# Optimization experiments

Measured on AMD Instinct MI355X. Metric: run time of the kernel, lower is better.

The kernel has to match this reference:

```python
import jax, jax.numpy as jnp
import numpy as np
import math

DIM = 4096
N_HEADS = 32
HEAD_DIM = DIM // N_HEADS  # 128


def setup_inputs() -> dict:
    key = jax.random.key(0)
    ks = jax.random.split(key, 10)
    B, S, C = 2, 1024, 2048
    x = jax.random.normal(ks[0], (B, S, DIM), dtype=jnp.float32)
    freqs_cis = jax.random.normal(ks[1], (S, HEAD_DIM // 2), dtype=jnp.float32)
    mask = jnp.zeros((1, 1, S, C), dtype=jnp.float32)
    input_idexes = jnp.arange(S, dtype=jnp.int64) if jax.config.jax_enable_x64 else jnp.arange(S, dtype=jnp.int32)
    cache_k = jax.random.normal(ks[2], (B, C, N_HEADS, HEAD_DIM), dtype=jnp.float32) * 0.1
    cache_v = jax.random.normal(ks[3], (B, C, N_HEADS, HEAD_DIM), dtype=jnp.float32) * 0.1
    # Linear weights in torch layout [out_features, in_features], y = x @ W.T
    wq = jax.random.normal(ks[4], (DIM, DIM), dtype=jnp.float32) * 0.02
    wk = jax.random.normal(ks[5], (DIM, DIM), dtype=jnp.float32) * 0.02
    wv = jax.random.normal(ks[6], (DIM, DIM), dtype=jnp.float32) * 0.02
    wo = jax.random.normal(ks[7], (DIM, DIM), dtype=jnp.float32) * 0.02
    return {"x": x, "freqs_cis": freqs_cis, "mask": mask, "input_idexes": input_idexes,
            "cache_k": cache_k, "cache_v": cache_v, "wq": wq, "wk": wk, "wv": wv, "wo": wo}


def reference(x, freqs_cis, mask, input_idexes, cache_k, cache_v, wq, wk, wv, wo):
    B, S, D = x.shape
    H, hd = N_HEADS, HEAD_DIM
    # projections (torch Linear: x @ W.T)
    xq = jnp.einsum('bsd,ed->bse', x, wq).reshape(B, S, H, hd)
    # xk/xv are computed in the original forward but never used (cache-only attention)
    xk = jnp.einsum('bsd,ed->bse', x, wk).reshape(B, S, H, hd)  # noqa: F841
    xv = jnp.einsum('bsd,ed->bse', x, wv).reshape(B, S, H, hd)  # noqa: F841
    q = xq.transpose(0, 2, 1, 3)                 # [B,H,S,hd]
    keys = cache_k.transpose(0, 2, 1, 3)         # [B,H,C,hd]
    values = cache_v.transpose(0, 2, 1, 3)       # [B,H,C,hd]
    scores = jnp.einsum('bhse,bhce->bhsc', q, keys) / math.sqrt(hd)
    scores = scores + mask
    attn = jax.nn.softmax(scores.astype(jnp.float32), axis=-1).astype(q.dtype)
    out = jnp.einsum('bhsc,bhce->bhse', attn, values)  # [B,H,S,hd]
    out = out.transpose(0, 2, 1, 3).reshape(B, S, H * hd)
    return jnp.einsum('bse,de->bsd', out, wo)
```

## Files before the change

kernel.cpp:

```cpp
#include <hip/hip_runtime.h>
#include <hip/hip_bf16.h>
#include <stdint.h>


#define DIM   4096
#define NH    32
#define HD    128
#define BB    2
#define SS    1024
#define CC    2048

typedef __bf16 bf16x8 __attribute__((ext_vector_type(8)));
typedef float  f32x4  __attribute__((ext_vector_type(4)));

__device__ __forceinline__ unsigned short f2bf(float f) {
  union { __hip_bfloat16 h; unsigned short u; } cv;
  cv.h = __float2bfloat16(f);
  return cv.u;
}

__device__ __forceinline__ void gl_lds16(const void* g, void* l) {
  __builtin_amdgcn_global_load_lds(
      (__attribute__((address_space(1))) void*)(uintptr_t)(g),
      (__attribute__((address_space(3))) void*)(l), 16, 0, 0);
}

__global__ void conv_f32_bf16(const float* __restrict__ in, unsigned short* __restrict__ out, int n4) {
  int i = blockIdx.x * blockDim.x + threadIdx.x;
  int stride = gridDim.x * blockDim.x;
  for (; i < n4; i += stride) {
    float4 v = reinterpret_cast<const float4*>(in)[i];
    ushort4 o;
    o.x = f2bf(v.x); o.y = f2bf(v.y); o.z = f2bf(v.z); o.w = f2bf(v.w);
    reinterpret_cast<ushort4*>(out)[i] = o;
  }
}

__global__ __launch_bounds__(256) void prep_a(
    const float* __restrict__ x,  unsigned short* __restrict__ xbf,
    const float* __restrict__ wq, unsigned short* __restrict__ wbf)
{
  const int b = blockIdx.x, t = threadIdx.x;
  const float* in; unsigned short* out; int base, nthr, n4;
  if (b < 1024) { in = x;  out = xbf; base = b;        nthr = 1024 * 256; n4 = BB * SS * DIM / 4; }
  else          { in = wq; out = wbf; base = b - 1024; nthr = 2048 * 256; n4 = DIM * DIM / 4; }
  for (int i = base * 256 + t; i < n4; i += nthr) {
    float4 v = reinterpret_cast<const float4*>(in)[i];
    ushort4 o;
    o.x = f2bf(v.x); o.y = f2bf(v.y); o.z = f2bf(v.z); o.w = f2bf(v.w);
    reinterpret_cast<ushort4*>(out)[i] = o;
  }
}

__global__ __launch_bounds__(256) void prep_b(
    const float* __restrict__ ck,  unsigned short* __restrict__ kbf,
    const float* __restrict__ cv,  unsigned short* __restrict__ vtbf,
    const float* __restrict__ mask, int* __restrict__ flags)
{
  const int b = blockIdx.x, t = threadIdx.x;

  if (b < 2048) {
    const int total4 = BB * NH * CC * HD / 4;
    for (int i = b * 256 + t; i < total4; i += 2048 * 256) {
      size_t o = (size_t)i * 4;
      int d  = (int)(o & (HD - 1));
      size_t r = o >> 7;
      int c  = (int)(r & (CC - 1));
      int bh = (int)(r >> 11);
      int hh = bh & (NH - 1), bb = bh >> 5;
      float4 v = *reinterpret_cast<const float4*>(ck + ((size_t)(bb * CC + c) * NH + hh) * HD + d);
      ushort4 u; u.x = f2bf(v.x); u.y = f2bf(v.y); u.z = f2bf(v.z); u.w = f2bf(v.w);
      *reinterpret_cast<ushort4*>(kbf + o) = u;
    }
  } else if (b < 6144) {
    __shared__ float tile[64][65];
    const int e  = b - 2048;
    const int ct = e & 31, rest = e >> 5;
    const int dt = rest & 1, bh = rest >> 1;
    const int hh = bh & (NH - 1), bb = bh >> 5;
    const int c0 = ct * 64, d0 = dt * 64;
    const int tx = t & 63, ty = t >> 6;
#pragma unroll
    for (int i = 0; i < 16; ++i) {
      int cl = ty + i * 4;
      tile[cl][tx] = cv[((size_t)(bb * CC + c0 + cl) * NH + hh) * HD + d0 + tx];
    }
    __syncthreads();
    const int c4 = (t & 15) * 4, dr = t >> 4;
#pragma unroll
    for (int i = 0; i < 4; ++i) {
      int dl = dr + i * 16;
      ushort4 o;
      o.x = f2bf(tile[c4 + 0][dl]); o.y = f2bf(tile[c4 + 1][dl]);
      o.z = f2bf(tile[c4 + 2][dl]); o.w = f2bf(tile[c4 + 3][dl]);
      *reinterpret_cast<ushort4*>(&vtbf[((size_t)bh * HD + d0 + dl) * CC + c0 + c4]) = o;
    }
  } else {
    __shared__ int s[4];
    const int e  = b - 6144;
    const int qt = e >> 5, ct = e & 31;
    const int w = t >> 6;
    const float4* m4 = (const float4*)mask;
    int nz = 0;
#pragma unroll
    for (int i = 0; i < 8; ++i) {
      int idx = i * 256 + t;
      int row = idx >> 4, c4 = idx & 15;
      float4 v = m4[(size_t)(qt * 128 + row) * (CC / 4) + ct * 16 + c4];
      nz |= (v.x != 0.f) | (v.y != 0.f) | (v.z != 0.f) | (v.w != 0.f);
    }
    int wa = (int)__any(nz);
    if ((t & 63) == 0) s[w] = wa;
    __syncthreads();
    if (t == 0) flags[qt * 32 + ct] = s[0] | s[1] | s[2] | s[3];
  }
}

template <int OUT_BF16>
__global__ __launch_bounds__(256, 2) void gemm_bt(
    const unsigned short* __restrict__ A,
    const unsigned short* __restrict__ Bw,
    void* __restrict__ Cout,
    int M, int N, int K, float scale)
{
  __shared__ __align__(16) unsigned short As[128 * 32];
  __shared__ __align__(16) unsigned short Bs[128 * 32];
  const int t = threadIdx.x;
  const int w = t >> 6, lane = t & 63;
  const int wr = w >> 1, wc = w & 1;
  const int bm0 = blockIdx.y * 128, bn0 = blockIdx.x * 128;

  const unsigned short* aSrc = A  + (size_t)(bm0 + (t >> 2)) * K + (t & 3) * 8;
  const unsigned short* bSrc = Bw + (size_t)(bn0 + (t >> 2)) * K + (t & 3) * 8;
  char* aDst = (char*)As + w * 1024;
  char* bDst = (char*)Bs + w * 1024;
  const size_t half = (size_t)64 * K;

  f32x4 acc[4][4];
#pragma unroll
  for (int m = 0; m < 4; ++m)
#pragma unroll
    for (int n = 0; n < 4; ++n) acc[m][n] = (f32x4){0.f, 0.f, 0.f, 0.f};

  for (int k0 = 0; k0 < K; k0 += 32) {
    gl_lds16(aSrc,        aDst);
    gl_lds16(aSrc + half, aDst + 4096);
    gl_lds16(bSrc,        bDst);
    gl_lds16(bSrc + half, bDst + 4096);
    aSrc += 32; bSrc += 32;
    __syncthreads();

    bf16x8 af[4], bf[4];
#pragma unroll
    for (int m = 0; m < 4; ++m)
      af[m] = *(const bf16x8*)&As[(wr * 64 + m * 16 + (lane & 15)) * 32 + (lane >> 4) * 8];
#pragma unroll
    for (int n = 0; n < 4; ++n)
      bf[n] = *(const bf16x8*)&Bs[(wc * 64 + n * 16 + (lane & 15)) * 32 + (lane >> 4) * 8];
#pragma unroll
    for (int m = 0; m < 4; ++m)
#pragma unroll
      for (int n = 0; n < 4; ++n)
        acc[m][n] = __builtin_amdgcn_mfma_f32_16x16x32_bf16(af[m], bf[n], acc[m][n], 0, 0, 0);
    __syncthreads();
  }

  const int r0 = (lane >> 4) * 4, cl = lane & 15;
#pragma unroll
  for (int m = 0; m < 4; ++m) {
#pragma unroll
    for (int n = 0; n < 4; ++n) {
      int row = bm0 + wr * 64 + m * 16 + r0;
      int col = bn0 + wc * 64 + n * 16 + cl;
#pragma unroll
      for (int r = 0; r < 4; ++r) {
        float v = acc[m][n][r] * scale;
        if (OUT_BF16) ((unsigned short*)Cout)[(size_t)(row + r) * N + col] = f2bf(v);
        else          ((float*)Cout)[(size_t)(row + r) * N + col] = v;
      }
    }
  }
}

__global__ __launch_bounds__(256, 2) void fused_qattn(
    const unsigned short* __restrict__ Ax,
    const unsigned short* __restrict__ Wq,
    const unsigned short* __restrict__ Kb,
    const unsigned short* __restrict__ Vtb,
    const float* __restrict__ mask,
    const int* __restrict__ Mf,
    unsigned short* __restrict__ Ob)
{
  __shared__ __align__(16) unsigned short SM[40960];

  const int t = threadIdx.x, w = t >> 6, lane = t & 63;
  const int lg = (blockIdx.x & 7) * 64 + (blockIdx.x >> 3);
  const int qt = lg & 7, bh = lg >> 3;
  const int hh = bh & (NH - 1), bb = bh >> 5;
  const int q0 = qt * 128;
  const int l15 = lane & 15, g = lane >> 4;
  const int rb4 = g * 4;
  const int wr = w >> 1, wc = w & 1;

  const int bm0 = bb * SS + q0;
  const int bn0 = hh * HD;
  {
    unsigned short* As = SM;
    unsigned short* Bs = SM + 4096;
    const unsigned short* aSrc = Ax + (size_t)(bm0 + (t >> 2)) * DIM + (t & 3) * 8;
    const unsigned short* bSrc = Wq + (size_t)(bn0 + (t >> 2)) * DIM + (t & 3) * 8;
    char* aDst = (char*)As + w * 1024;
    char* bDst = (char*)Bs + w * 1024;
    const size_t half = (size_t)64 * DIM;

    f32x4 acc[4][4];
#pragma unroll
    for (int m = 0; m < 4; ++m)
#pragma unroll
      for (int n = 0; n < 4; ++n) acc[m][n] = (f32x4){0.f, 0.f, 0.f, 0.f};

    for (int k0 = 0; k0 < DIM; k0 += 32) {
      gl_lds16(aSrc,        aDst);
      gl_lds16(aSrc + half, aDst + 4096);
      gl_lds16(bSrc,        bDst);
      gl_lds16(bSrc + half, bDst + 4096);
      aSrc += 32; bSrc += 32;
      __syncthreads();

      bf16x8 af[4], bf[4];
#pragma unroll
      for (int m = 0; m < 4; ++m)
        af[m] = *(const bf16x8*)&As[(wr * 64 + m * 16 + l15) * 32 + g * 8];
#pragma unroll
      for (int n = 0; n < 4; ++n)
        bf[n] = *(const bf16x8*)&Bs[(wc * 64 + n * 16 + l15) * 32 + g * 8];
#pragma unroll
      for (int m = 0; m < 4; ++m)
#pragma unroll
        for (int n = 0; n < 4; ++n)
          acc[m][n] = __builtin_amdgcn_mfma_f32_16x16x32_bf16(af[m], bf[n], acc[m][n], 0, 0, 0);
      __syncthreads();
    }

    const float qscale = 0.12751744682f;
    const int r0 = g * 4;
#pragma unroll
    for (int m = 0; m < 4; ++m) {
#pragma unroll
      for (int n = 0; n < 4; ++n) {
        int rl = wr * 64 + m * 16 + r0;
        int cl2 = wc * 64 + n * 16 + l15;
#pragma unroll
        for (int r = 0; r < 4; ++r) {
          int row = rl + r;
          SM[(row * 128 + cl2) ^ ((row & 7) << 3)] = f2bf(acc[m][n][r] * qscale);
        }
      }
    }
  }
  __syncthreads();

  const int swz = (lane & 7) << 3;
  bf16x8 qf[2][4];
#pragma unroll
  for (int rf = 0; rf < 2; ++rf) {
    int row = w * 32 + rf * 16 + l15;
#pragma unroll
    for (int kk = 0; kk < 4; ++kk)
      qf[rf][kk] = *(const bf16x8*)&SM[(row * 128 + kk * 32 + g * 8) ^ swz];
  }
  __syncthreads();

  unsigned short* PsW = SM + 32768 + w * 2048;

  const unsigned short* kSrc = Kb + ((size_t)bh * CC + (t >> 4)) * HD
                               + (((t & 15) ^ ((t >> 4) & 7)) * 8);
  const unsigned short* vSrc = Vtb + ((size_t)bh * HD + (t >> 3)) * CC
                               + (((t & 7) ^ ((t >> 3) & 7)) * 8);

  f32x4 acc_o[2][8];
#pragma unroll
  for (int rf = 0; rf < 2; ++rf)
#pragma unroll
    for (int i = 0; i < 8; ++i) acc_o[rf][i] = (f32x4){0.f, 0.f, 0.f, 0.f};
  float m_run[2][4], l_run[2][4];
#pragma unroll
  for (int rf = 0; rf < 2; ++rf)
#pragma unroll
    for (int r = 0; r < 4; ++r) { m_run[rf][r] = -1e30f; l_run[rf][r] = 0.f; }

  const float LOG2E = 1.4426950408889634f;

  int mflag = Mf[qt * 32];
  {
    char* kd = (char*)(SM)         + w * 1024;
    char* vd = (char*)(SM + 16384) + w * 1024;
#pragma unroll
    for (int i = 0; i < 4; ++i) {
      gl_lds16(kSrc + (size_t)(i * 16) * HD, kd + i * 4096);
      gl_lds16(vSrc + (size_t)i * 32 * CC,   vd + i * 4096);
    }
  }
  __syncthreads();

  int cur = 0;
  for (int c0 = 0; c0 < CC; c0 += 64) {
    const int ct = c0 >> 6;
    int nextFlag = (ct < 31) ? Mf[qt * 32 + ct + 1] : 0;
    unsigned short* KsC = SM + cur * 8192;
    unsigned short* VsC = SM + 16384 + cur * 8192;

    float mk[2][4][4];
    if (mflag) {
#pragma unroll
      for (int rf = 0; rf < 2; ++rf)
#pragma unroll
        for (int nf = 0; nf < 4; ++nf)
#pragma unroll
          for (int r = 0; r < 4; ++r)
            mk[rf][nf][r] = mask[(size_t)(q0 + w * 32 + rf * 16 + rb4 + r) * CC
                                 + c0 + nf * 16 + l15];
      __builtin_amdgcn_sched_barrier(0);
    }

    if (c0 + 64 < CC) {
      char* kd = (char*)(SM + (cur ^ 1) * 8192)         + w * 1024;
      char* vd = (char*)(SM + 16384 + (cur ^ 1) * 8192) + w * 1024;
#pragma unroll
      for (int i = 0; i < 4; ++i) {
        gl_lds16(kSrc + (size_t)(c0 + 64 + i * 16) * HD, kd + i * 4096);
        gl_lds16(vSrc + (size_t)i * 32 * CC + c0 + 64,   vd + i * 4096);
      }
    }
    __builtin_amdgcn_sched_barrier(0);

    f32x4 sc[2][4];
#pragma unroll
    for (int rf = 0; rf < 2; ++rf)
#pragma unroll
      for (int nf = 0; nf < 4; ++nf) sc[rf][nf] = (f32x4){0.f, 0.f, 0.f, 0.f};
    __builtin_amdgcn_s_setprio(1);
#pragma unroll
    for (int kk = 0; kk < 4; ++kk) {
#pragma unroll
      for (int nf = 0; nf < 4; ++nf) {
        bf16x8 kf = *(const bf16x8*)&KsC[((nf * 16 + l15) * 128 + kk * 32 + g * 8) ^ swz];
        sc[0][nf] = __builtin_amdgcn_mfma_f32_16x16x32_bf16(qf[0][kk], kf, sc[0][nf], 0, 0, 0);
        sc[1][nf] = __builtin_amdgcn_mfma_f32_16x16x32_bf16(qf[1][kk], kf, sc[1][nf], 0, 0, 0);
      }
    }
    __builtin_amdgcn_s_setprio(0);

    if (mflag) {
#pragma unroll
      for (int rf = 0; rf < 2; ++rf)
#pragma unroll
        for (int nf = 0; nf < 4; ++nf)
#pragma unroll
          for (int r = 0; r < 4; ++r)
            sc[rf][nf][r] = fmaf(mk[rf][nf][r], LOG2E, sc[rf][nf][r]);
    }

#pragma unroll
    for (int rf = 0; rf < 2; ++rf) {
      int ok = 1;
      float pm[4];
#pragma unroll
      for (int r = 0; r < 4; ++r) {
        pm[r] = fmaxf(fmaxf(sc[rf][0][r], sc[rf][1][r]), fmaxf(sc[rf][2][r], sc[rf][3][r]));
        ok = ok && (pm[r] <= m_run[rf][r] + 8.0f);
      }
      if (!__all(ok)) {
#pragma unroll
        for (int r = 0; r < 4; ++r) {
          float mx = pm[r];
#pragma unroll
          for (int d = 1; d < 16; d <<= 1)
            mx = fmaxf(mx, __shfl_xor(mx, d));
          float mn = fmaxf(m_run[rf][r], mx);
          float corr = __builtin_amdgcn_exp2f(m_run[rf][r] - mn);
          m_run[rf][r] = mn;
          l_run[rf][r] *= corr;
#pragma unroll
          for (int nd = 0; nd < 8; ++nd) acc_o[rf][nd][r] *= corr;
        }
      }

#pragma unroll
      for (int r = 0; r < 4; ++r) {
        int rw = rf * 16 + rb4 + r;
        int rsw = (rw & 7) << 3;
#pragma unroll
        for (int nf = 0; nf < 4; ++nf) {
          float p = __builtin_amdgcn_exp2f(sc[rf][nf][r] - m_run[rf][r]);
          l_run[rf][r] += p;
          PsW[rw * 64 + ((nf * 16 + l15) ^ rsw)] = f2bf(p);
        }
      }
    }

    __builtin_amdgcn_s_setprio(1);
#pragma unroll
    for (int kk = 0; kk < 2; ++kk) {
      bf16x8 pf0 = *(const bf16x8*)&PsW[((0 * 16 + l15) * 64 + kk * 32 + g * 8) ^ swz];
      bf16x8 pf1 = *(const bf16x8*)&PsW[((1 * 16 + l15) * 64 + kk * 32 + g * 8) ^ swz];
#pragma unroll
      for (int nd = 0; nd < 8; ++nd) {
        bf16x8 vf = *(const bf16x8*)&VsC[((nd * 16 + l15) * 64 + kk * 32 + g * 8) ^ swz];
        acc_o[0][nd] = __builtin_amdgcn_mfma_f32_16x16x32_bf16(pf0, vf, acc_o[0][nd], 0, 0, 0);
        acc_o[1][nd] = __builtin_amdgcn_mfma_f32_16x16x32_bf16(pf1, vf, acc_o[1][nd], 0, 0, 0);
      }
    }
    __builtin_amdgcn_s_setprio(0);
    __syncthreads();
    cur ^= 1;
    mflag = nextFlag;
  }

#pragma unroll
  for (int rf = 0; rf < 2; ++rf) {
#pragma unroll
    for (int r = 0; r < 4; ++r)
#pragma unroll
      for (int d = 1; d < 16; d <<= 1)
        l_run[rf][r] += __shfl_xor(l_run[rf][r], d);

#pragma unroll
    for (int nd = 0; nd < 8; ++nd)
#pragma unroll
      for (int r = 0; r < 4; ++r) {
        float v = acc_o[rf][nd][r] / l_run[rf][r];
        int row = q0 + w * 32 + rf * 16 + rb4 + r;
        Ob[(size_t)(bb * SS + row) * DIM + hh * HD + nd * 16 + l15] = f2bf(v);
      }
  }
}

extern "C" void kernel_launch(void* const* d_in, const int* in_sizes, int n_in,
                              void* d_out, int out_size, void* d_ws, size_t ws_size,
                              hipStream_t stream) {
  const float* x       = (const float*)d_in[0];
  const float* mask    = (const float*)d_in[2];
  const float* cache_k = (const float*)d_in[4];
  const float* cache_v = (const float*)d_in[5];
  const float* wq      = (const float*)d_in[6];
  const float* wo      = (const float*)d_in[9];
  float* out = (float*)d_out;

  char* ws = (char*)d_ws;
  unsigned short* Wbf  = (unsigned short*)(ws);
  unsigned short* xbf  = (unsigned short*)(ws + 33554432);
  unsigned short* qbf  = (unsigned short*)(ws + 33554432 + 16777216);
  unsigned short* kbf  = (unsigned short*)(ws + 33554432 + 2 * 16777216);
  unsigned short* vtbf = (unsigned short*)(ws + 2 * 33554432 + 2 * 16777216);
  int* mflags = (int*)d_out;

  prep_b<<<6400, 256, 0, stream>>>(cache_k, kbf, cache_v, vtbf, mask, mflags);
  prep_a<<<3072, 256, 0, stream>>>(x, xbf, wq, Wbf);
  fused_qattn<<<BB * NH * 8, 256, 0, stream>>>(xbf, Wbf, kbf, vtbf, mask, mflags, qbf);
  conv_f32_bf16<<<2048, 256, 0, stream>>>(wo, Wbf, DIM * DIM / 4);
  dim3 gg(DIM / 128, (BB * SS) / 128);
  gemm_bt<0><<<gg, 256, 0, stream>>>(qbf, Wbf, out, BB * SS, DIM, DIM, 1.0f);
}
```

Before: 345.7 us.

## Fuse fp32-to-bf16 conversion of x, wq and wo into GEMM tile loads

Drops the separate conversion kernels for x, wq and wo. The Q-projection and output GEMMs now stream fp32 tiles straight into LDS with an XOR swizzle and convert them to bf16 while building MFMA fragments. This removes two launches and the write and re-read of bf16 copies. In exchange the GEMM loops move twice the bytes from global memory and LDS per tile and do conversion work in the inner loop, and x and wq are re-read and re-converted by every tile that uses them.

New measurement: 453.2 us. +31.1%, slower.

```diff
diff --git a/kernel.cpp b/kernel.cpp
--- a/kernel.cpp
+++ b/kernel.cpp
@@ -25,31 +25,14 @@
       (__attribute__((address_space(3))) void*)(l), 16, 0, 0);
 }
 
-__global__ void conv_f32_bf16(const float* __restrict__ in, unsigned short* __restrict__ out, int n4) {
-  int i = blockIdx.x * blockDim.x + threadIdx.x;
-  int stride = gridDim.x * blockDim.x;
-  for (; i < n4; i += stride) {
-    float4 v = reinterpret_cast<const float4*>(in)[i];
-    ushort4 o;
-    o.x = f2bf(v.x); o.y = f2bf(v.y); o.z = f2bf(v.z); o.w = f2bf(v.w);
-    reinterpret_cast<ushort4*>(out)[i] = o;
-  }
-}
-
-__global__ __launch_bounds__(256) void prep_a(
-    const float* __restrict__ x,  unsigned short* __restrict__ xbf,
-    const float* __restrict__ wq, unsigned short* __restrict__ wbf)
-{
-  const int b = blockIdx.x, t = threadIdx.x;
-  const float* in; unsigned short* out; int base, nthr, n4;
-  if (b < 1024) { in = x;  out = xbf; base = b;        nthr = 1024 * 256; n4 = BB * SS * DIM / 4; }
-  else          { in = wq; out = wbf; base = b - 1024; nthr = 2048 * 256; n4 = DIM * DIM / 4; }
-  for (int i = base * 256 + t; i < n4; i += nthr) {
-    float4 v = reinterpret_cast<const float4*>(in)[i];
-    ushort4 o;
-    o.x = f2bf(v.x); o.y = f2bf(v.y); o.z = f2bf(v.z); o.w = f2bf(v.w);
-    reinterpret_cast<ushort4*>(out)[i] = o;
-  }
+__device__ __forceinline__ bf16x8 frag_from_f32(const char* base, int row, int g) {
+  const int s = row & 7;
+  f32x4 c0 = *(const f32x4*)(base + row * 128 + (((2 * g)    ) ^ s) * 16);
+  f32x4 c1 = *(const f32x4*)(base + row * 128 + (((2 * g) | 1) ^ s) * 16);
+  union { bf16x8 v; unsigned short u[8]; } r;
+  r.u[0] = f2bf(c0[0]); r.u[1] = f2bf(c0[1]); r.u[2] = f2bf(c0[2]); r.u[3] = f2bf(c0[3]);
+  r.u[4] = f2bf(c1[0]); r.u[5] = f2bf(c1[1]); r.u[6] = f2bf(c1[2]); r.u[7] = f2bf(c1[3]);
+  return r.v;
 }
 
 __global__ __launch_bounds__(256) void prep_b(
@@ -116,25 +99,24 @@
   }
 }
 
-template <int OUT_BF16>
-__global__ __launch_bounds__(256, 2) void gemm_bt(
+__global__ __launch_bounds__(256) void gemm_o(
     const unsigned short* __restrict__ A,
-    const unsigned short* __restrict__ Bw,
-    void* __restrict__ Cout,
-    int M, int N, int K, float scale)
+    const float* __restrict__ Bw,
+    float* __restrict__ Cout)
 {
   __shared__ __align__(16) unsigned short As[128 * 32];
-  __shared__ __align__(16) unsigned short Bs[128 * 32];
+  __shared__ __align__(16) float Bsf[128 * 32];
   const int t = threadIdx.x;
   const int w = t >> 6, lane = t & 63;
+  const int l15 = lane & 15, g = lane >> 4;
   const int wr = w >> 1, wc = w & 1;
   const int bm0 = blockIdx.y * 128, bn0 = blockIdx.x * 128;
 
-  const unsigned short* aSrc = A  + (size_t)(bm0 + (t >> 2)) * K + (t & 3) * 8;
-  const unsigned short* bSrc = Bw + (size_t)(bn0 + (t >> 2)) * K + (t & 3) * 8;
+  const unsigned short* aSrc = A + (size_t)(bm0 + (t >> 2)) * DIM + (t & 3) * 8;
+  const float* bSrc = Bw + (size_t)(bn0 + (t >> 3)) * DIM + ((t & 7) ^ ((t >> 3) & 7)) * 4;
   char* aDst = (char*)As + w * 1024;
-  char* bDst = (char*)Bs + w * 1024;
-  const size_t half = (size_t)64 * K;
+  char* bDst = (char*)Bsf + w * 1024;
+  const size_t halfA = (size_t)64 * DIM;
 
   f32x4 acc[4][4];
 #pragma unroll
@@ -142,21 +124,22 @@
 #pragma unroll
     for (int n = 0; n < 4; ++n) acc[m][n] = (f32x4){0.f, 0.f, 0.f, 0.f};
 
-  for (int k0 = 0; k0 < K; k0 += 32) {
-    gl_lds16(aSrc,        aDst);
-    gl_lds16(aSrc + half, aDst + 4096);
-    gl_lds16(bSrc,        bDst);
-    gl_lds16(bSrc + half, bDst + 4096);
+  for (int k0 = 0; k0 < DIM; k0 += 32) {
+    gl_lds16(aSrc,         aDst);
+    gl_lds16(aSrc + halfA, aDst + 4096);
+#pragma unroll
+    for (int i = 0; i < 4; ++i)
+      gl_lds16(bSrc + (size_t)(i * 32) * DIM, bDst + i * 4096);
     aSrc += 32; bSrc += 32;
     __syncthreads();
 
     bf16x8 af[4], bf[4];
 #pragma unroll
     for (int m = 0; m < 4; ++m)
-      af[m] = *(const bf16x8*)&As[(wr * 64 + m * 16 + (lane & 15)) * 32 + (lane >> 4) * 8];
+      af[m] = *(const bf16x8*)&As[(wr * 64 + m * 16 + l15) * 32 + g * 8];
 #pragma unroll
     for (int n = 0; n < 4; ++n)
-      bf[n] = *(const bf16x8*)&Bs[(wc * 64 + n * 16 + (lane & 15)) * 32 + (lane >> 4) * 8];
+      bf[n] = frag_from_f32((const char*)Bsf, wc * 64 + n * 16 + l15, g);
 #pragma unroll
     for (int m = 0; m < 4; ++m)
 #pragma unroll
@@ -165,26 +148,23 @@
     __syncthreads();
   }
 
-  const int r0 = (lane >> 4) * 4, cl = lane & 15;
+  const int r0 = g * 4;
 #pragma unroll
   for (int m = 0; m < 4; ++m) {
 #pragma unroll
     for (int n = 0; n < 4; ++n) {
       int row = bm0 + wr * 64 + m * 16 + r0;
-      int col = bn0 + wc * 64 + n * 16 + cl;
-#pragma unroll
-      for (int r = 0; r < 4; ++r) {
-        float v = acc[m][n][r] * scale;
-        if (OUT_BF16) ((unsigned short*)Cout)[(size_t)(row + r) * N + col] = f2bf(v);
-        else          ((float*)Cout)[(size_t)(row + r) * N + col] = v;
-      }
+      int col = bn0 + wc * 64 + n * 16 + l15;
+#pragma unroll
+      for (int r = 0; r < 4; ++r)
+        Cout[(size_t)(row + r) * DIM + col] = acc[m][n][r];
     }
   }
 }
 
 __global__ __launch_bounds__(256, 2) void fused_qattn(
-    const unsigned short* __restrict__ Ax,
-    const unsigned short* __restrict__ Wq,
+    const float* __restrict__ Xf,
+    const float* __restrict__ Wqf,
     const unsigned short* __restrict__ Kb,
     const unsigned short* __restrict__ Vtb,
     const float* __restrict__ mask,
@@ -205,13 +185,10 @@
   const int bm0 = bb * SS + q0;
   const int bn0 = hh * HD;
   {
-    unsigned short* As = SM;
-    unsigned short* Bs = SM + 4096;
-    const unsigned short* aSrc = Ax + (size_t)(bm0 + (t >> 2)) * DIM + (t & 3) * 8;
-    const unsigned short* bSrc = Wq + (size_t)(bn0 + (t >> 2)) * DIM + (t & 3) * 8;
-    char* aDst = (char*)As + w * 1024;
-    char* bDst = (char*)Bs + w * 1024;
-    const size_t half = (size_t)64 * DIM;
+    const float* aS = Xf  + (size_t)(bm0 + (t >> 3)) * DIM + ((t & 7) ^ ((t >> 3) & 7)) * 4;
+    const float* bS = Wqf + (size_t)(bn0 + (t >> 3)) * DIM + ((t & 7) ^ ((t >> 3) & 7)) * 4;
+    char* aDst = (char*)SM + w * 1024;
+    char* bDst = (char*)SM + 16384 + w * 1024;
 
     f32x4 acc[4][4];
 #pragma unroll
@@ -220,20 +197,21 @@
       for (int n = 0; n < 4; ++n) acc[m][n] = (f32x4){0.f, 0.f, 0.f, 0.f};
 
     for (int k0 = 0; k0 < DIM; k0 += 32) {
-      gl_lds16(aSrc,        aDst);
-      gl_lds16(aSrc + half, aDst + 4096);
-      gl_lds16(bSrc,        bDst);
-      gl_lds16(bSrc + half, bDst + 4096);
-      aSrc += 32; bSrc += 32;
+#pragma unroll
+      for (int i = 0; i < 4; ++i) {
+        gl_lds16(aS + (size_t)(i * 32) * DIM, aDst + i * 4096);
+        gl_lds16(bS + (size_t)(i * 32) * DIM, bDst + i * 4096);
+      }
+      aS += 32; bS += 32;
       __syncthreads();
 
       bf16x8 af[4], bf[4];
 #pragma unroll
       for (int m = 0; m < 4; ++m)
-        af[m] = *(const bf16x8*)&As[(wr * 64 + m * 16 + l15) * 32 + g * 8];
+        af[m] = frag_from_f32((const char*)SM, wr * 64 + m * 16 + l15, g);
 #pragma unroll
       for (int n = 0; n < 4; ++n)
-        bf[n] = *(const bf16x8*)&Bs[(wc * 64 + n * 16 + l15) * 32 + g * 8];
+        bf[n] = frag_from_f32((const char*)SM + 16384, wc * 64 + n * 16 + l15, g);
 #pragma unroll
       for (int m = 0; m < 4; ++m)
 #pragma unroll
@@ -448,17 +426,12 @@
   float* out = (float*)d_out;
 
   char* ws = (char*)d_ws;
-  unsigned short* Wbf  = (unsigned short*)(ws);
-  unsigned short* xbf  = (unsigned short*)(ws + 33554432);
-  unsigned short* qbf  = (unsigned short*)(ws + 33554432 + 16777216);
-  unsigned short* kbf  = (unsigned short*)(ws + 33554432 + 2 * 16777216);
-  unsigned short* vtbf = (unsigned short*)(ws + 2 * 33554432 + 2 * 16777216);
+  unsigned short* qbf  = (unsigned short*)(ws);
+  unsigned short* kbf  = (unsigned short*)(ws + 16777216);
+  unsigned short* vtbf = (unsigned short*)(ws + 16777216 + 33554432);
   int* mflags = (int*)d_out;
 
   prep_b<<<6400, 256, 0, stream>>>(cache_k, kbf, cache_v, vtbf, mask, mflags);
-  prep_a<<<3072, 256, 0, stream>>>(x, xbf, wq, Wbf);
-  fused_qattn<<<BB * NH * 8, 256, 0, stream>>>(xbf, Wbf, kbf, vtbf, mask, mflags, qbf);
-  conv_f32_bf16<<<2048, 256, 0, stream>>>(wo, Wbf, DIM * DIM / 4);
-  dim3 gg(DIM / 128, (BB * SS) / 128);
-  gemm_bt<0><<<gg, 256, 0, stream>>>(qbf, Wbf, out, BB * SS, DIM, DIM, 1.0f);
-}
+  fused_qattn<<<BB * NH * 8, 256, 0, stream>>>(x, wq, kbf, vtbf, mask, mflags, qbf);
+  gemm_o<<<dim3(DIM / 128, (BB * SS) / 128), 256, 0, stream>>>(qbf, wo, out);
+}
```
